# Performance work log

Hardware: AMD Instinct MI355X
Metric: run time of the kernel (lower is better)

The kernel has to match this reference:

```python
import jax, jax.numpy as jnp
import numpy as np

T, B, I, H = 1024, 32768, 1, 3  # time steps, batch, input size, hidden size (from nn.LSTM(1,3,1,...))


def setup_inputs() -> dict:
    key = jax.random.key(0)
    ks = jax.random.split(key, 7)
    return {
        "x": jax.random.normal(ks[0], (T, B, I), dtype=jnp.float32),
        "h0": jax.random.normal(ks[1], (B, H), dtype=jnp.float32),
        "c0": jax.random.normal(ks[2], (B, H), dtype=jnp.float32),
        "W_ih": jax.random.normal(ks[3], (4 * H, I), dtype=jnp.float32) * (1.0 / np.sqrt(H)),
        "W_hh": jax.random.normal(ks[4], (4 * H, H), dtype=jnp.float32) * (1.0 / np.sqrt(H)),
        "b_ih": jax.random.normal(ks[5], (4 * H,), dtype=jnp.float32) * (1.0 / np.sqrt(H)),
        "b_hh": jax.random.normal(ks[6], (4 * H,), dtype=jnp.float32) * (1.0 / np.sqrt(H)),
    }


def reference(x, h0, c0, W_ih, W_hh, b_ih, b_hh):
    """Sequential single-layer LSTM over T steps (PyTorch gate order i,f,g,o).

    x: [T, B, I]; returns hidden-state sequence ys: [T, B, H].
    """
    # Precompute input projection for all steps at once: [T, B, 4H]
    x_proj = jnp.einsum("tbi,gi->tbg", x, W_ih) + b_ih + b_hh

    def step(carry, xg):
        h, c = carry
        gates = xg + h @ W_hh.T  # [B, 4H]
        i_, f_, g_, o_ = jnp.split(gates, 4, axis=-1)
        c_new = jax.nn.sigmoid(f_) * c + jax.nn.sigmoid(i_) * jnp.tanh(g_)
        h_new = jax.nn.sigmoid(o_) * jnp.tanh(c_new)
        return (h_new, c_new), h_new

    (hn, cn), ys = jax.lax.scan(step, (h0, c0), x_proj)
    return ys
```

## Files before the change

kernel.cpp:

```cpp
#include <hip/hip_runtime.h>


constexpr int T_STEPS = 1024;
constexpr int BATCH   = 32768;
constexpr int HID     = 3;
constexpr int G4      = 4 * HID;
constexpr int NB      = 16;

__device__ __forceinline__ float fsigmoid(float z) {
    float e = __builtin_amdgcn_exp2f(-1.4426950408889634f * z);
    return __builtin_amdgcn_rcpf(1.0f + e);
}
__device__ __forceinline__ float ftanh(float z) {
    float e = __builtin_amdgcn_exp2f(2.8853900817779268f * z);
    return 1.0f - 2.0f * __builtin_amdgcn_rcpf(e + 1.0f);
}

__global__ __launch_bounds__(64) void lstm_seq_kernel(
    const float* __restrict__ x,
    const float* __restrict__ h0,
    const float* __restrict__ c0,
    const float* __restrict__ W_ih,
    const float* __restrict__ W_hh,
    const float* __restrict__ b_ih,
    const float* __restrict__ b_hh,
    float* __restrict__ out)
{
    const int b = blockIdx.x * blockDim.x + threadIdx.x;
    if (b >= BATCH) return;

    float wi[G4], bias[G4], wh[G4][HID];
#pragma unroll
    for (int r = 0; r < G4; ++r) {
        wi[r]   = W_ih[r];
        bias[r] = b_ih[r] + b_hh[r];
#pragma unroll
        for (int j = 0; j < HID; ++j) wh[r][j] = W_hh[r * HID + j];
    }

    float h[HID], c[HID];
#pragma unroll
    for (int j = 0; j < HID; ++j) {
        h[j] = h0[b * HID + j];
        c[j] = c0[b * HID + j];
    }

    float cur[NB], nxt[NB];
#pragma unroll
    for (int i = 0; i < NB; ++i) cur[i] = x[i * BATCH + b];

    for (int chunk = 0; chunk < T_STEPS / NB; ++chunk) {
        const int base_next = (chunk + 1) * NB;
#pragma unroll
        for (int i = 0; i < NB; ++i) {
            int tl = base_next + i;
            if (tl >= T_STEPS) tl = T_STEPS - 1;
            nxt[i] = x[tl * BATCH + b];
        }

#pragma unroll
        for (int i = 0; i < NB; ++i) {
            const int t = chunk * NB + i;
            const float xv = cur[i];

            float pre[G4];
#pragma unroll
            for (int r = 0; r < G4; ++r) {
                float v = fmaf(xv, wi[r], bias[r]);
                v = fmaf(h[0], wh[r][0], v);
                v = fmaf(h[1], wh[r][1], v);
                v = fmaf(h[2], wh[r][2], v);
                pre[r] = v;
            }

#pragma unroll
            for (int j = 0; j < HID; ++j) {
                float ig = fsigmoid(pre[j]);
                float fg = fsigmoid(pre[HID + j]);
                float gg = ftanh(pre[2 * HID + j]);
                float og = fsigmoid(pre[3 * HID + j]);
                c[j] = fmaf(fg, c[j], ig * gg);
                h[j] = og * ftanh(c[j]);
            }

            const int obase = (t * BATCH + b) * HID;
            out[obase + 0] = h[0];
            out[obase + 1] = h[1];
            out[obase + 2] = h[2];
        }

#pragma unroll
        for (int i = 0; i < NB; ++i) cur[i] = nxt[i];
    }
}

extern "C" void kernel_launch(void* const* d_in, const int* in_sizes, int n_in,
                              void* d_out, int out_size, void* d_ws, size_t ws_size,
                              hipStream_t stream) {
    const float* x    = (const float*)d_in[0];
    const float* h0   = (const float*)d_in[1];
    const float* c0   = (const float*)d_in[2];
    const float* W_ih = (const float*)d_in[3];
    const float* W_hh = (const float*)d_in[4];
    const float* b_ih = (const float*)d_in[5];
    const float* b_hh = (const float*)d_in[6];
    float* out = (float*)d_out;

    dim3 grid(BATCH / 64), block(64);
    lstm_seq_kernel<<<grid, block, 0, stream>>>(x, h0, c0, W_ih, W_hh, b_ih, b_hh, out);
}
```

Measured before the change: 701.6 us.

## Split each LSTM batch element across a quad of lanes with DPP broadcast

Each batch element is now handled by four lanes: three lanes each own one hidden unit and the fourth duplicates unit 0. Hidden state is shared within the quad each step using DPP quad_perm broadcasts. This cuts the serial per-thread dependency chain and raises thread-level parallelism, and output stores become contiguous across lanes for better coalescing. The cost is 4x threads, one wasted lane per quad, and redundant x loads and transcendental work.

```diff
diff --git a/kernel.cpp b/kernel.cpp
--- a/kernel.cpp
+++ b/kernel.cpp
@@ -4,7 +4,6 @@
 constexpr int T_STEPS = 1024;
 constexpr int BATCH   = 32768;
 constexpr int HID     = 3;
-constexpr int G4      = 4 * HID;
 constexpr int NB      = 16;
 
 __device__ __forceinline__ float fsigmoid(float z) {
@@ -16,7 +15,13 @@
     return 1.0f - 2.0f * __builtin_amdgcn_rcpf(e + 1.0f);
 }
 
-__global__ __launch_bounds__(64) void lstm_seq_kernel(
+template <int CTRL>
+__device__ __forceinline__ float qbcast(float v) {
+    return __int_as_float(
+        __builtin_amdgcn_update_dpp(0, __float_as_int(v), CTRL, 0xF, 0xF, true));
+}
+
+__global__ __launch_bounds__(256, 2) void lstm_quad_kernel(
     const float* __restrict__ x,
     const float* __restrict__ h0,
     const float* __restrict__ c0,
@@ -26,24 +31,25 @@
     const float* __restrict__ b_hh,
     float* __restrict__ out)
 {
-    const int b = blockIdx.x * blockDim.x + threadIdx.x;
-    if (b >= BATCH) return;
+    const int tid  = blockIdx.x * 256 + threadIdx.x;
+    const int lane = tid & 3;
+    const int b    = tid >> 2;
+    const int u    = (lane == 3) ? 0 : lane;
 
-    float wi[G4], bias[G4], wh[G4][HID];
+    float wiv[4], bv[4], w0[4], w1[4], w2[4];
 #pragma unroll
-    for (int r = 0; r < G4; ++r) {
-        wi[r]   = W_ih[r];
-        bias[r] = b_ih[r] + b_hh[r];
-#pragma unroll
-        for (int j = 0; j < HID; ++j) wh[r][j] = W_hh[r * HID + j];
+    for (int g = 0; g < 4; ++g) {
+        const int r = 3 * g + u;
+        wiv[g] = W_ih[r];
+        bv[g]  = b_ih[r] + b_hh[r];
+        w0[g]  = W_hh[r * HID + 0];
+        w1[g]  = W_hh[r * HID + 1];
+        w2[g]  = W_hh[r * HID + 2];
     }
 
-    float h[HID], c[HID];
-#pragma unroll
-    for (int j = 0; j < HID; ++j) {
-        h[j] = h0[b * HID + j];
-        c[j] = c0[b * HID + j];
-    }
+    float h = h0[b * HID + u];
+    float c = c0[b * HID + u];
+    const int obase = b * HID + u;
 
     float cur[NB], nxt[NB];
 #pragma unroll
@@ -60,33 +66,30 @@
 
 #pragma unroll
         for (int i = 0; i < NB; ++i) {
-            const int t = chunk * NB + i;
+            const int t  = chunk * NB + i;
             const float xv = cur[i];
 
-            float pre[G4];
-#pragma unroll
-            for (int r = 0; r < G4; ++r) {
-                float v = fmaf(xv, wi[r], bias[r]);
-                v = fmaf(h[0], wh[r][0], v);
-                v = fmaf(h[1], wh[r][1], v);
-                v = fmaf(h[2], wh[r][2], v);
-                pre[r] = v;
-            }
+            const float hv0 = qbcast<0x00>(h);
+            const float hv1 = qbcast<0x55>(h);
+            const float hv2 = qbcast<0xAA>(h);
 
-#pragma unroll
-            for (int j = 0; j < HID; ++j) {
-                float ig = fsigmoid(pre[j]);
-                float fg = fsigmoid(pre[HID + j]);
-                float gg = ftanh(pre[2 * HID + j]);
-                float og = fsigmoid(pre[3 * HID + j]);
-                c[j] = fmaf(fg, c[j], ig * gg);
-                h[j] = og * ftanh(c[j]);
-            }
+            float pi = fmaf(xv, wiv[0], bv[0]);
+            float pf = fmaf(xv, wiv[1], bv[1]);
+            float pg = fmaf(xv, wiv[2], bv[2]);
+            float po = fmaf(xv, wiv[3], bv[3]);
+            pi = fmaf(hv0, w0[0], pi); pi = fmaf(hv1, w1[0], pi); pi = fmaf(hv2, w2[0], pi);
+            pf = fmaf(hv0, w0[1], pf); pf = fmaf(hv1, w1[1], pf); pf = fmaf(hv2, w2[1], pf);
+            pg = fmaf(hv0, w0[2], pg); pg = fmaf(hv1, w1[2], pg); pg = fmaf(hv2, w2[2], pg);
+            po = fmaf(hv0, w0[3], po); po = fmaf(hv1, w1[3], po); po = fmaf(hv2, w2[3], po);
 
-            const int obase = (t * BATCH + b) * HID;
-            out[obase + 0] = h[0];
-            out[obase + 1] = h[1];
-            out[obase + 2] = h[2];
+            const float ig = fsigmoid(pi);
+            const float fg = fsigmoid(pf);
+            const float gg = ftanh(pg);
+            const float og = fsigmoid(po);
+            c = fmaf(fg, c, ig * gg);
+            h = og * ftanh(c);
+
+            if (lane < 3) out[t * (BATCH * HID) + obase] = h;
         }
 
 #pragma unroll
@@ -106,6 +109,6 @@
     const float* b_hh = (const float*)d_in[6];
     float* out = (float*)d_out;
 
-    dim3 grid(BATCH / 64), block(64);
-    lstm_seq_kernel<<<grid, block, 0, stream>>>(x, h0, c0, W_ih, W_hh, b_ih, b_hh, out);
+    dim3 grid((4 * BATCH) / 256), block(256);
+    lstm_quad_kernel<<<grid, block, 0, stream>>>(x, h0, c0, W_ih, W_hh, b_ih, b_hh, out);
 }
```

Result: faster. 616.3 us (-12.2%).
